# Performance work log

Measured on AMD Instinct MI355X. Metric: run time of the kernel, lower is better.

The kernel has to match this reference:

```python
import jax, jax.numpy as jnp
import numpy as np

D_MODEL = 1024
N_HEADS = 16
HEAD_DIM = D_MODEL // N_HEADS
NEG_INF = -1e10  # masked_fill value used in the original


def setup_inputs() -> dict:
    key = jax.random.key(0)
    ks = jax.random.split(key, 12)
    B, L = 2, 2048
    s = 0.02
    return {
        "query": jax.random.normal(ks[0], (B, L, D_MODEL), jnp.float32),
        "key": jax.random.normal(ks[1], (B, L, D_MODEL), jnp.float32),
        "value": jax.random.normal(ks[2], (B, L, D_MODEL), jnp.float32),
        "mask": jnp.ones((B, 1, L, L), jnp.int32),
        "Wq": jax.random.normal(ks[3], (D_MODEL, D_MODEL), jnp.float32) * s,
        "bq": jax.random.normal(ks[4], (D_MODEL,), jnp.float32) * s,
        "Wk": jax.random.normal(ks[5], (D_MODEL, D_MODEL), jnp.float32) * s,
        "bk": jax.random.normal(ks[6], (D_MODEL,), jnp.float32) * s,
        "Wv": jax.random.normal(ks[7], (D_MODEL, D_MODEL), jnp.float32) * s,
        "bv": jax.random.normal(ks[8], (D_MODEL,), jnp.float32) * s,
        "Wo": jax.random.normal(ks[9], (D_MODEL, D_MODEL), jnp.float32) * s,
        "bo": jax.random.normal(ks[10], (D_MODEL,), jnp.float32) * s,
    }


def _split_heads(x, B):
    # [B, L, D] -> [B, H, L, hd]
    return x.reshape(B, -1, N_HEADS, HEAD_DIM).transpose(0, 2, 1, 3)


def reference(query, key, value, mask, Wq, bq, Wk, bk, Wv, bv, Wo, bo):
    B = query.shape[0]
    scale = jnp.sqrt(jnp.asarray(HEAD_DIM, query.dtype))
    Q = _split_heads(query @ Wq + bq, B)   # [B,H,Lq,hd]
    K = _split_heads(key @ Wk + bk, B)     # [B,H,Lk,hd]
    V = _split_heads(value @ Wv + bv, B)   # [B,H,Lk,hd]
    energy = jnp.einsum('bhqd,bhkd->bhqk', Q, K) / scale
    energy = jnp.where(mask == 0, jnp.asarray(NEG_INF, energy.dtype), energy)
    # NOTE: the original applies softmax over dim=1 (the HEADS axis); replicated faithfully.
    attention = jax.nn.softmax(energy, axis=1)
    x = jnp.einsum('bhqk,bhkd->bhqd', attention, V)  # dropout is identity at inference
    x = x.transpose(0, 2, 1, 3).reshape(B, -1, D_MODEL)
    return x @ Wo + bo
```

## Files before the change

### kernel.cpp

```cpp
#include <hip/hip_runtime.h>
#include <hip/hip_bf16.h>
#include <stdint.h>

#define DM 1024
#define NH 16
#define HD 64
#define SEQ 2048
#define NB 2

typedef __attribute__((ext_vector_type(8)))  __bf16 bf16x8;
typedef __attribute__((ext_vector_type(4)))  __bf16 bf16x4;
typedef __attribute__((ext_vector_type(4)))  float  f32x4;
typedef __attribute__((ext_vector_type(16))) float  f32x16;
typedef __attribute__((ext_vector_type(4)))  unsigned int uint4v;

__device__ __forceinline__ f32x16 mfma32x32(bf16x8 a, bf16x8 b, f32x16 c) {
  return __builtin_amdgcn_mfma_f32_32x32x16_bf16(a, b, c, 0, 0, 0);
}
__device__ __forceinline__ f32x4 mfma16x16(bf16x8 a, bf16x8 b, f32x4 c) {
  return __builtin_amdgcn_mfma_f32_16x16x32_bf16(a, b, c, 0, 0, 0);
}
__device__ __forceinline__ unsigned pkbf(float a, float b) {
  unsigned short ua = __builtin_bit_cast(unsigned short, (__bf16)a);
  unsigned short ub = __builtin_bit_cast(unsigned short, (__bf16)b);
  return (unsigned)ua | ((unsigned)ub << 16);
}
__device__ __forceinline__ f32x16 zero16() {
  f32x16 z;
#pragma unroll
  for (int i = 0; i < 16; i++) z[i] = 0.0f;
  return z;
}

__global__ void wconv_kernel(const float* __restrict__ Wq, const float* __restrict__ Wk,
                             const float* __restrict__ Wv, const float* __restrict__ Wo,
                             __bf16* __restrict__ Wt) {
  __shared__ float tile[32][33];
  const int which = blockIdx.z;
  const float* W = (which == 0) ? Wq : (which == 1) ? Wk : (which == 2) ? Wv : Wo;
  __bf16* out = Wt + (size_t)which * DM * DM;
  const int n0 = blockIdx.x * 32, k0 = blockIdx.y * 32;
  const int tx = threadIdx.x & 31, ty = threadIdx.x >> 5;
#pragma unroll
  for (int i = 0; i < 4; i++) {
    tile[ty + i * 8][tx] = W[(size_t)(k0 + ty + i * 8) * DM + n0 + tx];
  }
  __syncthreads();
#pragma unroll
  for (int i = 0; i < 4; i++) {
    out[(size_t)(n0 + ty + i * 8) * DM + k0 + tx] = (__bf16)tile[tx][ty + i * 8];
  }
}

template <int AMODE, int OMODE>
__global__ __launch_bounds__(256, 2)
void gemm_kernel(const void* __restrict__ Aptr, const void* __restrict__ A2ptr,
                 const __bf16* __restrict__ Bt, const float* __restrict__ bias,
                 void* __restrict__ Out) {
  __shared__ __bf16 Alds[128][40];
  __shared__ __bf16 Blds[128][40];
  const int tid = threadIdx.x;
  const int l = tid & 63, w = tid >> 6;
  const int wm = w >> 1, wn = w & 1;
  const int r0 = blockIdx.x * 128, c0 = blockIdx.y * 128;

  f32x4 acc[4][4];
#pragma unroll
  for (int m = 0; m < 4; m++)
#pragma unroll
    for (int n = 0; n < 4; n++)
#pragma unroll
      for (int r = 0; r < 4; r++) acc[m][n][r] = 0.0f;

  const int ar = tid >> 2;
  const int aq = tid & 3;
  const int br = tid >> 1;
  const int bh = tid & 1;

  for (int kt = 0; kt < DM / 32; kt++) {
#pragma unroll
    for (int rep = 0; rep < 2; rep++) {
      const int row = ar + rep * 64;
      float fv[8];
      if constexpr (AMODE == 0) {
        const float* src = (const float*)Aptr + (size_t)(r0 + row) * DM + kt * 32 + aq * 8;
        const f32x4 v0 = *(const f32x4*)(src);
        const f32x4 v1 = *(const f32x4*)(src + 4);
#pragma unroll
        for (int i = 0; i < 4; i++) { fv[i] = v0[i]; fv[4 + i] = v1[i]; }
      } else {
        const int rr = r0 + row; const int bb = rr >> 11; const int ll = rr & 2047;
        const int cc = kt * 32 + aq * 8; const int h = cc >> 6; const int d = cc & 63;
        const size_t off = (((size_t)bb * NH + h) * SEQ + ll) * HD + d;
        const f32x4 a0 = *(const f32x4*)((const float*)Aptr + off);
        const f32x4 a1 = *(const f32x4*)((const float*)Aptr + off + 4);
        const f32x4 b0 = *(const f32x4*)((const float*)A2ptr + off);
        const f32x4 b1 = *(const f32x4*)((const float*)A2ptr + off + 4);
#pragma unroll
        for (int i = 0; i < 4; i++) { fv[i] = a0[i] + b0[i]; fv[4 + i] = a1[i] + b1[i]; }
      }
      bf16x8 av;
#pragma unroll
      for (int i = 0; i < 8; i++) av[i] = (__bf16)fv[i];
      *(bf16x8*)&Alds[row][aq * 8] = av;
    }
    {
      const __bf16* bsrc = Bt + (size_t)(c0 + br) * DM + kt * 32 + bh * 16;
      bf16x8 v0 = *(const bf16x8*)bsrc;
      bf16x8 v1 = *(const bf16x8*)(bsrc + 8);
      *(bf16x8*)&Blds[br][bh * 16] = v0;
      *(bf16x8*)&Blds[br][bh * 16 + 8] = v1;
    }
    __syncthreads();
    bf16x8 af[4], bfr[4];
#pragma unroll
    for (int m = 0; m < 4; m++)
      af[m] = *(const bf16x8*)&Alds[wm * 64 + m * 16 + (l & 15)][(l >> 4) * 8];
#pragma unroll
    for (int n = 0; n < 4; n++)
      bfr[n] = *(const bf16x8*)&Blds[wn * 64 + n * 16 + (l & 15)][(l >> 4) * 8];
#pragma unroll
    for (int m = 0; m < 4; m++)
#pragma unroll
      for (int n = 0; n < 4; n++) acc[m][n] = mfma16x16(af[m], bfr[n], acc[m][n]);
    __syncthreads();
  }

  const int ccol = l & 15;
  const int crb = (l >> 4) * 4;
#pragma unroll
  for (int n = 0; n < 4; n++) {
    const int col = c0 + wn * 64 + n * 16 + ccol;
    const float bv = bias[col];
#pragma unroll
    for (int m = 0; m < 4; m++) {
      const int row = r0 + wm * 64 + m * 16 + crb;
      f32x4 v = acc[m][n];
#pragma unroll
      for (int r = 0; r < 4; r++) v[r] += bv;
      if constexpr (OMODE == 2) {
        float* O = (float*)Out;
#pragma unroll
        for (int r = 0; r < 4; r++) O[(size_t)(row + r) * DM + col] = v[r];
      } else if constexpr (OMODE == 0) {
        __bf16* O = (__bf16*)Out;
        const int h = col >> 6, d = col & 63;
#pragma unroll
        for (int r = 0; r < 4; r++) {
          const int rr = row + r; const int bb = rr >> 11; const int ll = rr & 2047;
          O[(((size_t)bb * NH + h) * SEQ + ll) * HD + d] = (__bf16)v[r];
        }
      } else {
        __bf16* O = (__bf16*)Out;
        const int h = col >> 6, d = col & 63;
        const int bb = row >> 11, ll = row & 2047;
        bf16x4 pk;
#pragma unroll
        for (int r = 0; r < 4; r++) pk[r] = (__bf16)v[r];
        *(bf16x4*)&O[(((size_t)bb * NH + h) * HD + d) * SEQ + ll] = pk;
      }
    }
  }
}

__device__ __forceinline__ void process_head(const float (&pp)[16], const float (&rd)[16],
                                             int hi, int lq, int k0,
                                             const __bf16* __restrict__ vbase,
                                             f32x16& x0, f32x16& x1) {
  unsigned u[8];
#pragma unroll
  for (int j = 0; j < 8; j++) {
    const float a = pp[2 * j] * rd[2 * j];
    const float b = pp[2 * j + 1] * rd[2 * j + 1];
    u[j] = pkbf(a, b);
  }
  unsigned t[8];
#pragma unroll
  for (int j = 0; j < 8; j++) t[j] = (unsigned)__shfl_xor((int)u[j], 32, 64);
  const unsigned w0 = hi ? t[2] : u[0];
  const unsigned w1 = hi ? t[3] : u[1];
  const unsigned w2 = hi ? u[2] : t[0];
  const unsigned w3 = hi ? u[3] : t[1];
  const unsigned w4 = hi ? t[6] : u[4];
  const unsigned w5 = hi ? t[7] : u[5];
  const unsigned w6 = hi ? u[6] : t[4];
  const unsigned w7 = hi ? u[7] : t[5];
  const uint4v s0v = {w0, w1, w2, w3};
  const uint4v s1v = {w4, w5, w6, w7};
  const bf16x8 pa0 = __builtin_bit_cast(bf16x8, s0v);
  const bf16x8 pa1 = __builtin_bit_cast(bf16x8, s1v);
  const __bf16* vp = vbase + (size_t)lq * SEQ + k0 + hi * 8;
  bf16x8 vf;
  vf = *(const bf16x8*)(vp);                     x0 = mfma32x32(pa0, vf, x0);
  vf = *(const bf16x8*)(vp + 16);                x0 = mfma32x32(pa1, vf, x0);
  vf = *(const bf16x8*)(vp + (size_t)32 * SEQ);  x1 = mfma32x32(pa0, vf, x1);
  vf = *(const bf16x8*)(vp + (size_t)32 * SEQ + 16); x1 = mfma32x32(pa1, vf, x1);
}

__global__ __launch_bounds__(512, 2)
void attn_kernel(const __bf16* __restrict__ Qh, const __bf16* __restrict__ Kh,
                 const __bf16* __restrict__ Vt, const int* __restrict__ mask,
                 float* __restrict__ Xp) {
  __shared__ float part[8 * 64 * 16];
  __shared__ float Dbuf[1024];
  __shared__ float biasl[32 * 34];
  const int tid = threadIdx.x;
  const int l = tid & 63;
  const int w = tid >> 6;
  const int lq = l & 31;
  const int hi = l >> 5;
  const int qt = blockIdx.x, b = blockIdx.y, c = blockIdx.z;
  const int q0 = qt * 32;
  const int h0 = w * 2;

  bf16x8 qf[2][4];
#pragma unroll
  for (int hh = 0; hh < 2; hh++) {
    const __bf16* qp = Qh + (((size_t)b * NH + h0 + hh) * SEQ + q0 + lq) * HD + hi * 8;
#pragma unroll
    for (int ch = 0; ch < 4; ch++) qf[hh][ch] = *(const bf16x8*)(qp + ch * 16);
  }
  f32x16 xacc[2][2];
#pragma unroll
  for (int i = 0; i < 2; i++)
#pragma unroll
    for (int j = 0; j < 2; j++) xacc[i][j] = zero16();

  const __bf16* kbase0 = Kh + ((size_t)b * NH + h0) * SEQ * HD;
  const __bf16* kbase1 = Kh + ((size_t)b * NH + h0 + 1) * SEQ * HD;
  const __bf16* vbase0 = Vt + ((size_t)b * NH + h0) * HD * SEQ;
  const __bf16* vbase1 = Vt + ((size_t)b * NH + h0 + 1) * HD * SEQ;

  for (int kt = 0; kt < 32; kt++) {
    const int k0 = c * 1024 + kt * 32;
    {
      const int qq = tid >> 4;
      const int kk = (tid & 15) * 2;
      const int* mp = mask + ((size_t)b * SEQ + q0 + qq) * SEQ + k0 + kk;
      const int m0 = mp[0], m1 = mp[1];
      biasl[qq * 34 + kk] = m0 ? 0.0f : -1e10f;
      biasl[qq * 34 + kk + 1] = m1 ? 0.0f : -1e10f;
    }
    __syncthreads();

    f32x16 e0 = zero16(), e1 = zero16();
#pragma unroll
    for (int ch = 0; ch < 4; ch++) {
      const bf16x8 kf = *(const bf16x8*)(kbase0 + ((size_t)(k0 + lq)) * HD + ch * 16 + hi * 8);
      e0 = mfma32x32(kf, qf[0][ch], e0);
    }
#pragma unroll
    for (int ch = 0; ch < 4; ch++) {
      const bf16x8 kf = *(const bf16x8*)(kbase1 + ((size_t)(k0 + lq)) * HD + ch * 16 + hi * 8);
      e1 = mfma32x32(kf, qf[1][ch], e1);
    }
    float p0[16], p1[16], s4[16];
#pragma unroll
    for (int r = 0; r < 16; r++) {
      const int crow = (r & 3) + 8 * (r >> 2) + 4 * hi;
      const float bv = biasl[lq * 34 + crow];
      const float a0 = fmaf(e0[r], 0.125f, bv);
      const float a1 = fmaf(e1[r], 0.125f, bv);
      p0[r] = __expf(a0);
      p1[r] = __expf(a1);
      s4[r] = p0[r] + p1[r];
    }
    {
      float* pw = &part[(unsigned)((w << 6) | l) * 16];
#pragma unroll
      for (int i = 0; i < 4; i++) {
        f32x4 v;
#pragma unroll
        for (int j = 0; j < 4; j++) v[j] = s4[4 * i + j];
        *(f32x4*)(pw + 4 * i) = v;
      }
    }
    __syncthreads();
    {
      const int p2 = tid * 2;
      float da = 0.0f, db = 0.0f;
#pragma unroll
      for (int w2 = 0; w2 < 8; w2++) {
        da += part[w2 * 1024 + p2];
        db += part[w2 * 1024 + p2 + 1];
      }
      Dbuf[p2] = da;
      Dbuf[p2 + 1] = db;
    }
    __syncthreads();
    float rd[16];
#pragma unroll
    for (int i = 0; i < 4; i++) {
      const f32x4 dv = *(const f32x4*)&Dbuf[l * 16 + i * 4];
#pragma unroll
      for (int j = 0; j < 4; j++) rd[4 * i + j] = __builtin_amdgcn_rcpf(dv[j]);
    }
    process_head(p0, rd, hi, lq, k0, vbase0, xacc[0][0], xacc[0][1]);
    process_head(p1, rd, hi, lq, k0, vbase1, xacc[1][0], xacc[1][1]);
  }

#pragma unroll
  for (int hh = 0; hh < 2; hh++) {
    float* xo = Xp + (size_t)c * ((size_t)NB * NH * SEQ * HD) +
                (((size_t)b * NH + h0 + hh) * SEQ + q0) * HD;
#pragma unroll
    for (int dt = 0; dt < 2; dt++) {
#pragma unroll
      for (int r = 0; r < 16; r++) {
        const int crow = (r & 3) + 8 * (r >> 2) + 4 * hi;
        xo[(size_t)crow * HD + dt * 32 + lq] = xacc[hh][dt][r];
      }
    }
  }
}

extern "C" void kernel_launch(void* const* d_in, const int* in_sizes, int n_in,
                              void* d_out, int out_size, void* d_ws, size_t ws_size,
                              hipStream_t stream) {
  const float* q = (const float*)d_in[0];
  const float* k = (const float*)d_in[1];
  const float* v = (const float*)d_in[2];
  const int* msk = (const int*)d_in[3];
  const float* Wq = (const float*)d_in[4];
  const float* bq = (const float*)d_in[5];
  const float* Wk = (const float*)d_in[6];
  const float* bk = (const float*)d_in[7];
  const float* Wv = (const float*)d_in[8];
  const float* bv = (const float*)d_in[9];
  const float* Wo = (const float*)d_in[10];
  const float* bo = (const float*)d_in[11];

  char* ws = (char*)d_ws;
  const size_t MB = 1024 * 1024;
  if (ws_size < 64 * MB) return;
  __bf16* Wt = (__bf16*)(ws);
  __bf16* Qh = (__bf16*)(ws + 8 * MB);
  __bf16* Kh = (__bf16*)(ws + 16 * MB);
  __bf16* Vt = (__bf16*)(ws + 24 * MB);
  float* Xp = (float*)(ws + 32 * MB);
  const size_t XCH = (size_t)NB * NH * SEQ * HD;

  wconv_kernel<<<dim3(32, 32, 4), 256, 0, stream>>>(Wq, Wk, Wv, Wo, Wt);
  gemm_kernel<0, 0><<<dim3(32, 8), 256, 0, stream>>>(q, nullptr, Wt, bq, Qh);
  gemm_kernel<0, 0><<<dim3(32, 8), 256, 0, stream>>>(k, nullptr, Wt + (size_t)DM * DM, bk, Kh);
  gemm_kernel<0, 1><<<dim3(32, 8), 256, 0, stream>>>(v, nullptr, Wt + (size_t)2 * DM * DM, bv, Vt);
  attn_kernel<<<dim3(64, 2, 2), 512, 0, stream>>>(Qh, Kh, Vt, msk, Xp);
  gemm_kernel<1, 2><<<dim3(32, 8), 256, 0, stream>>>(Xp, Xp + XCH, Wt + (size_t)3 * DM * DM, bo, d_out);
}
```

Measured before the change: 479.0 us.

## Fuse QKV GEMMs, split attention keys four ways, bitpack mask, bf16 partials

```diff
diff --git a/kernel.cpp b/kernel.cpp
--- a/kernel.cpp
+++ b/kernel.cpp
@@ -7,12 +7,15 @@
 #define HD 64
 #define SEQ 2048
 #define NB 2
+#define NC 4
+#define KCH (SEQ / NC)
 
 typedef __attribute__((ext_vector_type(8)))  __bf16 bf16x8;
 typedef __attribute__((ext_vector_type(4)))  __bf16 bf16x4;
 typedef __attribute__((ext_vector_type(4)))  float  f32x4;
 typedef __attribute__((ext_vector_type(16))) float  f32x16;
 typedef __attribute__((ext_vector_type(4)))  unsigned int uint4v;
+typedef __attribute__((ext_vector_type(4)))  int    i32x4;
 
 __device__ __forceinline__ f32x16 mfma32x32(bf16x8 a, bf16x8 b, f32x16 c) {
   return __builtin_amdgcn_mfma_f32_32x32x16_bf16(a, b, c, 0, 0, 0);
@@ -52,13 +55,19 @@
   }
 }
 
-template <int AMODE, int OMODE>
-__global__ __launch_bounds__(256, 2)
-void gemm_kernel(const void* __restrict__ Aptr, const void* __restrict__ A2ptr,
-                 const __bf16* __restrict__ Bt, const float* __restrict__ bias,
-                 void* __restrict__ Out) {
+__global__ __launch_bounds__(256, 3)
+void qkv_kernel(const float* __restrict__ Aq, const float* __restrict__ Ak,
+                const float* __restrict__ Av, const __bf16* __restrict__ Wt,
+                const float* __restrict__ bqv, const float* __restrict__ bkv,
+                const float* __restrict__ bvv, __bf16* __restrict__ Qh,
+                __bf16* __restrict__ Kh, __bf16* __restrict__ Vt) {
   __shared__ __bf16 Alds[128][40];
   __shared__ __bf16 Blds[128][40];
+  const int z = blockIdx.z;
+  const float* A = (z == 0) ? Aq : (z == 1) ? Ak : Av;
+  const __bf16* Bt = Wt + (size_t)z * DM * DM;
+  const float* bias = (z == 0) ? bqv : (z == 1) ? bkv : bvv;
+
   const int tid = threadIdx.x;
   const int l = tid & 63, w = tid >> 6;
   const int wm = w >> 1, wn = w & 1;
@@ -81,27 +90,12 @@
 #pragma unroll
     for (int rep = 0; rep < 2; rep++) {
       const int row = ar + rep * 64;
-      float fv[8];
-      if constexpr (AMODE == 0) {
-        const float* src = (const float*)Aptr + (size_t)(r0 + row) * DM + kt * 32 + aq * 8;
-        const f32x4 v0 = *(const f32x4*)(src);
-        const f32x4 v1 = *(const f32x4*)(src + 4);
-#pragma unroll
-        for (int i = 0; i < 4; i++) { fv[i] = v0[i]; fv[4 + i] = v1[i]; }
-      } else {
-        const int rr = r0 + row; const int bb = rr >> 11; const int ll = rr & 2047;
-        const int cc = kt * 32 + aq * 8; const int h = cc >> 6; const int d = cc & 63;
-        const size_t off = (((size_t)bb * NH + h) * SEQ + ll) * HD + d;
-        const f32x4 a0 = *(const f32x4*)((const float*)Aptr + off);
-        const f32x4 a1 = *(const f32x4*)((const float*)Aptr + off + 4);
-        const f32x4 b0 = *(const f32x4*)((const float*)A2ptr + off);
-        const f32x4 b1 = *(const f32x4*)((const float*)A2ptr + off + 4);
-#pragma unroll
-        for (int i = 0; i < 4; i++) { fv[i] = a0[i] + b0[i]; fv[4 + i] = a1[i] + b1[i]; }
-      }
+      const float* src = A + (size_t)(r0 + row) * DM + kt * 32 + aq * 8;
+      const f32x4 v0 = *(const f32x4*)(src);
+      const f32x4 v1 = *(const f32x4*)(src + 4);
       bf16x8 av;
 #pragma unroll
-      for (int i = 0; i < 8; i++) av[i] = (__bf16)fv[i];
+      for (int i = 0; i < 4; i++) { av[i] = (__bf16)v0[i]; av[4 + i] = (__bf16)v1[i]; }
       *(bf16x8*)&Alds[row][aq * 8] = av;
     }
     {
@@ -128,36 +122,30 @@
 
   const int ccol = l & 15;
   const int crb = (l >> 4) * 4;
+  __bf16* Ohm = (z == 0) ? Qh : Kh;
 #pragma unroll
   for (int n = 0; n < 4; n++) {
     const int col = c0 + wn * 64 + n * 16 + ccol;
     const float bv = bias[col];
+    const int h = col >> 6, d = col & 63;
 #pragma unroll
     for (int m = 0; m < 4; m++) {
       const int row = r0 + wm * 64 + m * 16 + crb;
       f32x4 v = acc[m][n];
 #pragma unroll
       for (int r = 0; r < 4; r++) v[r] += bv;
-      if constexpr (OMODE == 2) {
-        float* O = (float*)Out;
-#pragma unroll
-        for (int r = 0; r < 4; r++) O[(size_t)(row + r) * DM + col] = v[r];
-      } else if constexpr (OMODE == 0) {
-        __bf16* O = (__bf16*)Out;
-        const int h = col >> 6, d = col & 63;
+      if (z < 2) {
 #pragma unroll
         for (int r = 0; r < 4; r++) {
           const int rr = row + r; const int bb = rr >> 11; const int ll = rr & 2047;
-          O[(((size_t)bb * NH + h) * SEQ + ll) * HD + d] = (__bf16)v[r];
+          Ohm[(((size_t)bb * NH + h) * SEQ + ll) * HD + d] = (__bf16)v[r];
         }
       } else {
-        __bf16* O = (__bf16*)Out;
-        const int h = col >> 6, d = col & 63;
         const int bb = row >> 11, ll = row & 2047;
         bf16x4 pk;
 #pragma unroll
         for (int r = 0; r < 4; r++) pk[r] = (__bf16)v[r];
-        *(bf16x4*)&O[(((size_t)bb * NH + h) * HD + d) * SEQ + ll] = pk;
+        *(bf16x4*)&Vt[(((size_t)bb * NH + h) * HD + d) * SEQ + ll] = pk;
       }
     }
   }
@@ -191,19 +179,19 @@
   const bf16x8 pa1 = __builtin_bit_cast(bf16x8, s1v);
   const __bf16* vp = vbase + (size_t)lq * SEQ + k0 + hi * 8;
   bf16x8 vf;
-  vf = *(const bf16x8*)(vp);                     x0 = mfma32x32(pa0, vf, x0);
-  vf = *(const bf16x8*)(vp + 16);                x0 = mfma32x32(pa1, vf, x0);
-  vf = *(const bf16x8*)(vp + (size_t)32 * SEQ);  x1 = mfma32x32(pa0, vf, x1);
+  vf = *(const bf16x8*)(vp);                         x0 = mfma32x32(pa0, vf, x0);
+  vf = *(const bf16x8*)(vp + 16);                    x0 = mfma32x32(pa1, vf, x0);
+  vf = *(const bf16x8*)(vp + (size_t)32 * SEQ);      x1 = mfma32x32(pa0, vf, x1);
   vf = *(const bf16x8*)(vp + (size_t)32 * SEQ + 16); x1 = mfma32x32(pa1, vf, x1);
 }
 
-__global__ __launch_bounds__(512, 2)
+__global__ __launch_bounds__(512, 4)
 void attn_kernel(const __bf16* __restrict__ Qh, const __bf16* __restrict__ Kh,
                  const __bf16* __restrict__ Vt, const int* __restrict__ mask,
-                 float* __restrict__ Xp) {
+                 __bf16* __restrict__ Xp) {
   __shared__ float part[8 * 64 * 16];
   __shared__ float Dbuf[1024];
-  __shared__ float biasl[32 * 34];
+  __shared__ unsigned mbits[32 * 17];
   const int tid = threadIdx.x;
   const int l = tid & 63;
   const int w = tid >> 6;
@@ -213,6 +201,22 @@
   const int q0 = qt * 32;
   const int h0 = w * 2;
 
+  {
+    const int qq = tid >> 4, wi = tid & 15;
+    const i32x4* mp = (const i32x4*)(mask + ((size_t)b * SEQ + q0 + qq) * SEQ +
+                                     (size_t)c * KCH + wi * 32);
+    unsigned word = 0;
+#pragma unroll
+    for (int j = 0; j < 8; j++) {
+      const i32x4 v = mp[j];
+      word |= (v.x ? 1u : 0u) << (4 * j);
+      word |= (v.y ? 1u : 0u) << (4 * j + 1);
+      word |= (v.z ? 1u : 0u) << (4 * j + 2);
+      word |= (v.w ? 1u : 0u) << (4 * j + 3);
+    }
+    mbits[qq * 17 + wi] = word;
+  }
+
   bf16x8 qf[2][4];
 #pragma unroll
   for (int hh = 0; hh < 2; hh++) {
@@ -231,17 +235,10 @@
   const __bf16* vbase0 = Vt + ((size_t)b * NH + h0) * HD * SEQ;
   const __bf16* vbase1 = Vt + ((size_t)b * NH + h0 + 1) * HD * SEQ;
 
-  for (int kt = 0; kt < 32; kt++) {
-    const int k0 = c * 1024 + kt * 32;
-    {
-      const int qq = tid >> 4;
-      const int kk = (tid & 15) * 2;
-      const int* mp = mask + ((size_t)b * SEQ + q0 + qq) * SEQ + k0 + kk;
-      const int m0 = mp[0], m1 = mp[1];
-      biasl[qq * 34 + kk] = m0 ? 0.0f : -1e10f;
-      biasl[qq * 34 + kk + 1] = m1 ? 0.0f : -1e10f;
-    }
-    __syncthreads();
+  __syncthreads();
+
+  for (int kt = 0; kt < KCH / 32; kt++) {
+    const int k0 = c * KCH + kt * 32;
 
     f32x16 e0 = zero16(), e1 = zero16();
 #pragma unroll
@@ -254,11 +251,12 @@
       const bf16x8 kf = *(const bf16x8*)(kbase1 + ((size_t)(k0 + lq)) * HD + ch * 16 + hi * 8);
       e1 = mfma32x32(kf, qf[1][ch], e1);
     }
+    const unsigned mword = mbits[lq * 17 + kt];
     float p0[16], p1[16], s4[16];
 #pragma unroll
     for (int r = 0; r < 16; r++) {
       const int crow = (r & 3) + 8 * (r >> 2) + 4 * hi;
-      const float bv = biasl[lq * 34 + crow];
+      const float bv = ((mword >> crow) & 1u) ? 0.0f : -1e10f;
       const float a0 = fmaf(e0[r], 0.125f, bv);
       const float a1 = fmaf(e1[r], 0.125f, bv);
       p0[r] = __expf(a0);
@@ -299,17 +297,98 @@
     process_head(p1, rd, hi, lq, k0, vbase1, xacc[1][0], xacc[1][1]);
   }
 
+  const size_t XCH = (size_t)NB * NH * SEQ * HD;
 #pragma unroll
   for (int hh = 0; hh < 2; hh++) {
-    float* xo = Xp + (size_t)c * ((size_t)NB * NH * SEQ * HD) +
-                (((size_t)b * NH + h0 + hh) * SEQ + q0) * HD;
+    __bf16* xo = Xp + (size_t)c * XCH +
+                 (((size_t)b * NH + h0 + hh) * SEQ + q0) * HD;
 #pragma unroll
     for (int dt = 0; dt < 2; dt++) {
 #pragma unroll
       for (int r = 0; r < 16; r++) {
         const int crow = (r & 3) + 8 * (r >> 2) + 4 * hi;
-        xo[(size_t)crow * HD + dt * 32 + lq] = xacc[hh][dt][r];
+        xo[(size_t)crow * HD + dt * 32 + lq] = (__bf16)xacc[hh][dt][r];
       }
+    }
+  }
+}
+
+__global__ __launch_bounds__(256, 4)
+void ogemm_kernel(const __bf16* __restrict__ Xp, const __bf16* __restrict__ Bt,
+                  const float* __restrict__ bias, float* __restrict__ Out) {
+  __shared__ __bf16 Alds[64][40];
+  __shared__ __bf16 Blds[128][40];
+  const int tid = threadIdx.x;
+  const int l = tid & 63, w = tid >> 6;
+  const int r0 = blockIdx.x * 64, c0 = blockIdx.y * 128;
+
+  f32x4 acc[4][2];
+#pragma unroll
+  for (int m = 0; m < 4; m++)
+#pragma unroll
+    for (int n = 0; n < 2; n++)
+#pragma unroll
+      for (int r = 0; r < 4; r++) acc[m][n][r] = 0.0f;
+
+  const int ar = tid >> 2, aq = tid & 3;
+  const int br = tid >> 1, bh = tid & 1;
+  const size_t PART = (size_t)NB * NH * SEQ * HD;
+  const int rr = r0 + ar;
+  const int bb = rr >> 11, ll = rr & 2047;
+
+  for (int kt = 0; kt < DM / 32; kt++) {
+    {
+      const int cc = kt * 32 + aq * 8;
+      const int h = cc >> 6, d = cc & 63;
+      const size_t off = (((size_t)bb * NH + h) * SEQ + ll) * HD + d;
+      float fv[8];
+#pragma unroll
+      for (int i = 0; i < 8; i++) fv[i] = 0.0f;
+#pragma unroll
+      for (int c = 0; c < NC; c++) {
+        const bf16x8 v = *(const bf16x8*)(Xp + (size_t)c * PART + off);
+#pragma unroll
+        for (int i = 0; i < 8; i++) fv[i] += (float)v[i];
+      }
+      bf16x8 av;
+#pragma unroll
+      for (int i = 0; i < 8; i++) av[i] = (__bf16)fv[i];
+      *(bf16x8*)&Alds[ar][aq * 8] = av;
+    }
+    {
+      const __bf16* bsrc = Bt + (size_t)(c0 + br) * DM + kt * 32 + bh * 16;
+      bf16x8 v0 = *(const bf16x8*)bsrc;
+      bf16x8 v1 = *(const bf16x8*)(bsrc + 8);
+      *(bf16x8*)&Blds[br][bh * 16] = v0;
+      *(bf16x8*)&Blds[br][bh * 16 + 8] = v1;
+    }
+    __syncthreads();
+    bf16x8 af[4], bfr[2];
+#pragma unroll
+    for (int m = 0; m < 4; m++)
+      af[m] = *(const bf16x8*)&Alds[m * 16 + (l & 15)][(l >> 4) * 8];
+#pragma unroll
+    for (int n = 0; n < 2; n++)
+      bfr[n] = *(const bf16x8*)&Blds[w * 32 + n * 16 + (l & 15)][(l >> 4) * 8];
+#pragma unroll
+    for (int m = 0; m < 4; m++)
+#pragma unroll
+      for (int n = 0; n < 2; n++) acc[m][n] = mfma16x16(af[m], bfr[n], acc[m][n]);
+    __syncthreads();
+  }
+
+  const int ccol = l & 15;
+  const int crb = (l >> 4) * 4;
+#pragma unroll
+  for (int n = 0; n < 2; n++) {
+    const int col = c0 + w * 32 + n * 16 + ccol;
+    const float bv = bias[col];
+#pragma unroll
+    for (int m = 0; m < 4; m++) {
+      const int row = r0 + m * 16 + crb;
+      f32x4 v = acc[m][n];
+#pragma unroll
+      for (int r = 0; r < 4; r++) Out[(size_t)(row + r) * DM + col] = v[r] + bv;
     }
   }
 }
@@ -337,13 +416,10 @@
   __bf16* Qh = (__bf16*)(ws + 8 * MB);
   __bf16* Kh = (__bf16*)(ws + 16 * MB);
   __bf16* Vt = (__bf16*)(ws + 24 * MB);
-  float* Xp = (float*)(ws + 32 * MB);
-  const size_t XCH = (size_t)NB * NH * SEQ * HD;
+  __bf16* Xp = (__bf16*)(ws + 32 * MB);
 
   wconv_kernel<<<dim3(32, 32, 4), 256, 0, stream>>>(Wq, Wk, Wv, Wo, Wt);
-  gemm_kernel<0, 0><<<dim3(32, 8), 256, 0, stream>>>(q, nullptr, Wt, bq, Qh);
-  gemm_kernel<0, 0><<<dim3(32, 8), 256, 0, stream>>>(k, nullptr, Wt + (size_t)DM * DM, bk, Kh);
-  gemm_kernel<0, 1><<<dim3(32, 8), 256, 0, stream>>>(v, nullptr, Wt + (size_t)2 * DM * DM, bv, Vt);
-  attn_kernel<<<dim3(64, 2, 2), 512, 0, stream>>>(Qh, Kh, Vt, msk, Xp);
-  gemm_kernel<1, 2><<<dim3(32, 8), 256, 0, stream>>>(Xp, Xp + XCH, Wt + (size_t)3 * DM * DM, bo, d_out);
-}
+  qkv_kernel<<<dim3(32, 8, 3), 256, 0, stream>>>(q, k, v, Wt, bq, bk, bv, Qh, Kh, Vt);
+  attn_kernel<<<dim3(64, 2, NC), 512, 0, stream>>>(Qh, Kh, Vt, msk, Xp);
+  ogemm_kernel<<<dim3(64, 8), 256, 0, stream>>>(Xp, Wt + (size_t)3 * DM * DM, bo, (float*)d_out);
+}
```

After: 518.8 us. 8.3% more time.
